# Kernel optimization log

Hardware: AMD Instinct MI355X
Metric: run time of the kernel (lower is better)

## Reference

```python
import jax, jax.numpy as jnp
import numpy as np

N = 50000          # nodes
E = 1_600_000      # edges (avg degree 32)
F = 64             # num_features == hidden dim of every layer
R = 5              # num_rel (edge ratings)
B = 4              # num_base (basis decomposition)
L = 4              # number of RGCN layers (dim=[64,64,64,64])
K = 2048           # nodes with x[:,0]==1 (target user/item nodes)


def setup_inputs() -> dict:
    key = jax.random.key(0)
    ks = jax.random.split(key, 10)
    x = jax.random.normal(ks[0], (N, F), dtype=jnp.float32)
    target_idx = jnp.arange(K, dtype=jnp.int32)
    # mark exactly K target nodes: x[:,0] == 1 iff node index < K
    col0 = (jnp.arange(N) < K).astype(jnp.float32)
    x = x.at[:, 0].set(col0)
    edge_index = jax.random.randint(ks[1], (2, E), 0, N, dtype=jnp.int32)
    edge_type = jax.random.randint(ks[2], (E,), 0, R, dtype=jnp.int32)
    s = 1.0 / np.sqrt(F)
    bases = jax.random.normal(ks[3], (L, B, F, F), dtype=jnp.float32) * s
    comps = jax.random.normal(ks[4], (L, R, B), dtype=jnp.float32) * (1.0 / np.sqrt(B))
    roots = jax.random.normal(ks[5], (L, F, F), dtype=jnp.float32) * s
    biases = jnp.zeros((L, F), dtype=jnp.float32)
    w1 = jax.random.normal(ks[6], (2 * L * F, 128), dtype=jnp.float32) * (1.0 / np.sqrt(2 * L * F))
    b1 = jnp.zeros((128,), dtype=jnp.float32)
    w2 = jax.random.normal(ks[7], (128, 1), dtype=jnp.float32) * (1.0 / np.sqrt(128))
    b2 = jnp.zeros((1,), dtype=jnp.float32)
    return {"x": x, "edge_index": edge_index, "edge_type": edge_type,
            "target_idx": target_idx, "bases": bases, "comps": comps,
            "roots": roots, "biases": biases, "w1": w1, "b1": b1,
            "w2": w2, "b2": b2}


def _rgcn_layer(x, src, dst, etype, bases_l, comp_l, root_l, bias_l):
    # basis decomposition: W_r = sum_b comp[r,b] * bases[b]   -> [R, in, out]
    W = jnp.einsum('rb,bio->rio', comp_l, bases_l)
    # transform every node under every relation, then gather per edge
    H = jnp.einsum('ni,rio->rno', x, W)          # [R, N, out]
    m = H[etype, src]                            # [E, out] per-edge messages
    # per-(target node, relation) MEAN aggregation (PyG RGCNConv semantics)
    seg = dst * R + etype                        # [E]
    sums = jax.ops.segment_sum(m, seg, num_segments=N * R)
    cnts = jax.ops.segment_sum(jnp.ones((m.shape[0],), dtype=x.dtype), seg,
                               num_segments=N * R)
    mean = sums / jnp.maximum(cnts, 1.0)[:, None]
    agg = mean.reshape(N, R, -1).sum(axis=1)     # sum over relations
    return agg + x @ root_l + bias_l


def reference(x, edge_index, edge_type, target_idx, bases, comps, roots,
              biases, w1, b1, w2, b2):
    # inference mode: edge dropout / feature dropout are identity
    src, dst = edge_index[0], edge_index[1]
    h = x
    h_i = []
    for l in range(L):
        h = jnp.tanh(_rgcn_layer(h, src, dst, edge_type,
                                 bases[l], comps[l], roots[l], biases[l]))
        h_i.append(h)
    h_cat = jnp.concatenate(h_i, axis=1)         # [N, sum(dim)] = [N, 256]
    # u and i masks are identical in the source (x[:,0]==1); target_idx holds
    # exactly those node indices, so index gather == boolean mask selection.
    sel = h_cat[target_idx]                      # [K, 256]
    feat = jnp.concatenate([sel, sel], axis=1)   # [K, 512]
    hid = jax.nn.relu(feat @ w1 + b1)
    out = hid @ w2 + b2
    return out[:, 0]
```

## Files before the change

kernel.cpp:

```cpp
#include <hip/hip_runtime.h>
#include <hip/hip_bf16.h>

#define Nn 50000
#define Ee 1600000
#define Ff 64
#define Rr 5
#define Bb 4
#define Ll 4
#define Kk 2048
#define NBK 196
#define SEGB 1280
#define MsegP (NBK*SEGB)
#define NT32 1563
#define NCH ((Ee+8191)/8192)
#define WTSL (12*4*64*8)

typedef __attribute__((ext_vector_type(8))) short short8;
typedef __attribute__((ext_vector_type(4))) float v4f;

static __device__ __forceinline__ unsigned short f2b(float f){
  unsigned u = __float_as_uint(f);
  unsigned r = (u + 0x7fffu + ((u>>16)&1u)) >> 16;
  return (unsigned short)r;
}
static __device__ __forceinline__ unsigned packbf(float lo, float hi){
  return (unsigned)f2b(lo) | ((unsigned)f2b(hi) << 16);
}
static __device__ __forceinline__ float2 unpackbf(unsigned u){
  return make_float2(__uint_as_float(u << 16), __uint_as_float(u & 0xffff0000u));
}
static __device__ __forceinline__ void acc8(float* A, uint4 g){
  float2 f;
  f=unpackbf(g.x); A[0]+=f.x; A[1]+=f.y;
  f=unpackbf(g.y); A[2]+=f.x; A[3]+=f.y;
  f=unpackbf(g.z); A[4]+=f.x; A[5]+=f.y;
  f=unpackbf(g.w); A[6]+=f.x; A[7]+=f.y;
}

#define GATH4(B, MR) { \
  int i0 = __shfl((int)(MR), grp8 + ((B)&7) + 0, 64); \
  int i1 = __shfl((int)(MR), grp8 + ((B)&7) + 1, 64); \
  int i2 = __shfl((int)(MR), grp8 + ((B)&7) + 2, 64); \
  int i3 = __shfl((int)(MR), grp8 + ((B)&7) + 3, 64); \
  i0 = ((B)+0 < deg) ? i0 : Nn; \
  i1 = ((B)+1 < deg) ? i1 : Nn; \
  i2 = ((B)+2 < deg) ? i2 : Nn; \
  i3 = ((B)+3 < deg) ? i3 : Nn; \
  uint4 g0 = *(const uint4*)&h2[(size_t)i0*32 + li*4]; \
  uint4 g1 = *(const uint4*)&h2[(size_t)i1*32 + li*4]; \
  uint4 g2 = *(const uint4*)&h2[(size_t)i2*32 + li*4]; \
  uint4 g3 = *(const uint4*)&h2[(size_t)i3*32 + li*4]; \
  acc8(A, g0); acc8(A, g1); acc8(A, g2); acc8(A, g3); }

static __device__ __forceinline__ void seg_gather(int s, int deg, unsigned m0, unsigned m1,
    float* A, int grp8, int li, const unsigned short* __restrict__ srcs,
    const unsigned* __restrict__ h2)
{
  int dmax = deg;
  dmax = max(dmax, __shfl_xor(dmax, 8, 64));
  dmax = max(dmax, __shfl_xor(dmax, 16, 64));
  dmax = max(dmax, __shfl_xor(dmax, 32, 64));
  GATH4(0, m0)
  if (dmax > 4)  GATH4(4, m0)
  if (dmax > 8)  GATH4(8, m1)
  if (dmax > 12) GATH4(12, m1)
  if (dmax > 16){
    for (int j = 16; j < dmax; j++){
      unsigned u = srcs[s + j];
      int id = (j < deg) ? (int)u : Nn;
      uint4 g = *(const uint4*)&h2[(size_t)id*32 + li*4];
      acc8(A, g);
    }
  }
}

#define XB_B 6250
#define IV_B (XB_B+196)
#define WE_B (IV_B+128)
#define WS_B (WE_B+48)
#define TF_B (WS_B+7)
__global__ __launch_bounds__(256) void k_setupA(const float* __restrict__ x, unsigned* __restrict__ xb,
    int* __restrict__ inv, const float* __restrict__ w1, float* __restrict__ w1e,
    const float* __restrict__ bases, const float* __restrict__ comps, const float* __restrict__ roots,
    unsigned short* __restrict__ WTs, int* __restrict__ t32f, int* __restrict__ bcnt,
    unsigned* __restrict__ hA, unsigned* __restrict__ hB)
{
  int b = blockIdx.x, t = threadIdx.x;
  if (b < XB_B){
    int idx = b*256 + t;
    int n = idx >> 5, j = idx & 31;
    float2 v = *(const float2*)&x[(size_t)n*64 + 2*j];
    xb[idx] = packbf(v.x, v.y);
  } else if (b < IV_B){
    int i = (b-XB_B)*256 + t;
    if (i < Nn) inv[i] = -1;
  } else if (b < WE_B){
    int idx = (b-IV_B)*256 + t;
    int i = idx >> 7, j = idx & 127;
    w1e[idx] = w1[i*128 + j] + w1[(i+256)*128 + j];
  } else if (b < WS_B){
    int gid = (b-WE_B)*256 + t;
    int lane = gid & 63, nb = (gid>>6)&3, idx2 = gid>>8;
    int l = idx2/12, kk = idx2 - l*12;
    int o = nb*16 + (lane & 15);
    int kbase = kk*32 + (lane>>4)*8;
    const float* basesl = bases + (size_t)l*Bb*Ff*Ff;
    const float* compsl = comps + (size_t)l*Rr*Bb;
    const float* rootsl = roots + (size_t)l*Ff*Ff;
    unsigned short* wp = WTs + (size_t)gid*8;
    #pragma unroll
    for (int j=0;j<8;j++){
      int k = kbase + j;
      float s;
      if (k < 320){
        int c = k >> 6, i = k & 63;
        s = 0.f;
        #pragma unroll
        for (int bb2=0;bb2<Bb;bb2++)
          s += compsl[c*Bb+bb2] * basesl[(bb2*Ff + i)*Ff + o];
      } else {
        s = rootsl[(k-320)*Ff + o];
      }
      wp[j] = f2b(s);
    }
  } else if (b < TF_B){
    int i = (b-WS_B)*256 + t;
    if (i < NT32) t32f[i] = 0;
  } else {
    if (t < NBK+1) bcnt[t] = 0;
    if (t < 32){
      xb[(size_t)Nn*32 + t] = 0;
      hA[(size_t)Nn*32 + t] = 0;
      hB[(size_t)Nn*32 + t] = 0;
    }
  }
}

__global__ __launch_bounds__(256) void k_setupB(const int* __restrict__ tidx, int* __restrict__ inv,
                                                int* __restrict__ t32f){
  int k = blockIdx.x*256+threadIdx.x;
  if (k < Kk){
    int n = tidx[k];
    inv[n] = k;
    t32f[n >> 5] = 1;
  }
}

__global__ __launch_bounds__(256) void k_bcnt(const int* __restrict__ ei, int* __restrict__ bcnt){
  __shared__ int h[NBK];
  int t = threadIdx.x;
  for (int i=t;i<NBK;i+=256) h[i]=0;
  __syncthreads();
  int base = blockIdx.x*8192;
  for (int i=0;i<32;i++){
    int e = base + i*256 + t;
    if (e < Ee) atomicAdd(&h[ei[Ee+e]>>8], 1);
  }
  __syncthreads();
  for (int i=t;i<NBK;i+=256) if (h[i]) atomicAdd(&bcnt[i], h[i]);
}

__global__ __launch_bounds__(256) void k_bscan(const int* __restrict__ bcnt, int* __restrict__ bbase,
                                               int* __restrict__ bfill, int* __restrict__ rowptr){
  __shared__ int s[256];
  int t = threadIdx.x;
  int v = (t < NBK) ? bcnt[t] : 0;
  s[t] = v; __syncthreads();
  #pragma unroll
  for (int off=1; off<256; off<<=1){
    int x = (t>=off) ? s[t-off] : 0;
    __syncthreads();
    s[t] += x;
    __syncthreads();
  }
  if (t < NBK){ int ex = s[t]-v; bbase[t]=ex; bfill[t]=ex; }
  if (t == 0){ bbase[NBK] = Ee; rowptr[MsegP] = Ee; }
}

__global__ __launch_bounds__(256) void k_bin(const int* __restrict__ ei, const int* __restrict__ et,
                                             int* __restrict__ bfill, unsigned* __restrict__ ebin){
  __shared__ unsigned led[8192];
  __shared__ int h[NBK], gb[NBK];
  int t = threadIdx.x;
  for (int i=t;i<NBK;i+=256) h[i]=0;
  __syncthreads();
  int base = blockIdx.x*8192;
  for (int i=0;i<32;i++){
    int e = base + i*256 + t;
    if (e < Ee){
      int src = ei[e];
      int dst = ei[Ee+e];
      int r = et[e];
      led[i*256+t] = (unsigned)src | ((unsigned)(dst&255)<<16) | ((unsigned)r<<24);
      atomicAdd(&h[dst>>8], 1);
    }
  }
  __syncthreads();
  for (int i=t;i<NBK;i+=256) if (h[i]){ gb[i] = atomicAdd(&bfill[i], h[i]); h[i] = 0; }
  __syncthreads();
  for (int i=0;i<32;i++){
    int e = base + i*256 + t;
    if (e < Ee){
      int b = ei[Ee+e]>>8;
      int off = atomicAdd(&h[b], 1);
      ebin[gb[b]+off] = led[i*256+t];
    }
  }
}

__global__ __launch_bounds__(512) void k_sort(const unsigned* __restrict__ ebin, const int* __restrict__ bbase,
                                              unsigned short* __restrict__ srcs, int* __restrict__ rowptr){
  __shared__ int cntA[SEGB], excA[SEGB];
  int b = blockIdx.x, t = threadIdx.x;
  int base = bbase[b], cnt = bbase[b+1]-base;
  for (int i=t;i<SEGB;i+=512) cntA[i]=0;
  __syncthreads();
  for (int i=t;i<cnt;i+=512){
    unsigned u = ebin[base+i];
    int segl = (int)((u>>24)&7u)*256 + (int)((u>>16)&255u);
    atomicAdd(&cntA[segl], 1);
  }
  __syncthreads();
  for (int i=t;i<SEGB;i+=512) excA[i]=cntA[i];
  __syncthreads();
  for (int off=1; off<SEGB; off<<=1){
    int i0=t, i1=t+512, i2=t+1024;
    int v0 = (i0>=off)? excA[i0-off] : 0;
    int v1 = (i1>=off)? excA[i1-off] : 0;
    int v2 = (i2<SEGB && i2>=off)? excA[i2-off] : 0;
    __syncthreads();
    excA[i0]+=v0;
    excA[i1]+=v1;
    if (i2<SEGB) excA[i2]+=v2;
    __syncthreads();
  }
  for (int i=t;i<SEGB;i+=512){
    int ex = excA[i]-cntA[i];
    excA[i] = ex;
    rowptr[b*SEGB+i] = base + ex;
    cntA[i] = 0;
  }
  __syncthreads();
  for (int i=t;i<cnt;i+=512){
    unsigned u = ebin[base+i];
    int segl = (int)((u>>24)&7u)*256 + (int)((u>>16)&255u);
    int off = atomicAdd(&cntA[segl], 1);
    srcs[base + excA[segl] + off] = (unsigned short)(u & 0xffffu);
  }
}

__global__ __launch_bounds__(256, 4) void k_fused(const unsigned short* __restrict__ srcs,
    const int* __restrict__ rowptr, const unsigned* __restrict__ h2,
    const unsigned short* __restrict__ WTsl, const float* __restrict__ bias,
    unsigned short* __restrict__ hn, const int* __restrict__ inv, float* __restrict__ sel,
    int layer, const int* __restrict__ t32f)
{
  if (layer == Ll-1 && t32f[blockIdx.x] == 0) return;
  __shared__ __align__(16) unsigned short ytile[5*32*64];
  char* yb = (char*)ytile;
  int tid = threadIdx.x;
  int grp = tid >> 3;
  int li  = tid & 7;
  int grp8 = (tid & 63) & 56;
  int d0 = blockIdx.x * 32;
  int segbase = (d0 >> 8)*SEGB + (d0 & 255) + grp;

  int p[Rr], dg[Rr];
  #pragma unroll
  for (int r=0;r<Rr;r++){
    p[r]  = rowptr[segbase + r*256];
    dg[r] = rowptr[segbase + r*256 + 1] - p[r];
  }
  unsigned b0[Rr], b1[Rr];
  #pragma unroll
  for (int r=0;r<Rr;r++){
    b0[r] = srcs[p[r] + li];
    b1[r] = srcs[p[r] + 8 + li];
  }

  #pragma unroll
  for (int r=0;r<Rr;r++){
    int deg = dg[r];
    float A[8] = {0.f,0.f,0.f,0.f,0.f,0.f,0.f,0.f};
    seg_gather(p[r], deg, b0[r], b1[r], A, grp8, li, srcs, h2);
    float sc = (deg > 0) ? 1.0f/(float)deg : 0.f;
    uint4 o;
    o.x = packbf(A[0]*sc, A[1]*sc);
    o.y = packbf(A[2]*sc, A[3]*sc);
    o.z = packbf(A[4]*sc, A[5]*sc);
    o.w = packbf(A[6]*sc, A[7]*sc);
    int tr = r*32 + grp;
    *(uint4*)(yb + ((tr*128 + li*16) ^ ((tr&7)<<4))) = o;
  }
  __syncthreads();

  int wv = tid >> 6;
  int lane = tid & 63;
  int m = lane & 15, q = lane >> 4;
  const unsigned short* wp = WTsl + (size_t)lane*8 + (size_t)wv*512;
  const char* h2c = (const char*)h2;
  int row0 = d0 + m, row1 = d0 + 16 + m;
  int row0c = (row0 < Nn) ? row0 : Nn-1;
  int row1c = (row1 < Nn) ? row1 : Nn-1;
  v4f acc0 = {0.f,0.f,0.f,0.f}, acc1 = {0.f,0.f,0.f,0.f};
  #pragma unroll
  for (int kk=0; kk<12; kk++){
    short8 a0, a1;
    if (kk < 10){
      int rb = (kk>>1)*32;
      a0 = *(const short8*)(yb + (((rb+m   )*128 + (kk&1)*64 + q*16) ^ ((m&7)<<4)));
      a1 = *(const short8*)(yb + (((rb+16+m)*128 + (kk&1)*64 + q*16) ^ ((m&7)<<4)));
    } else {
      a0 = *(const short8*)(h2c + (size_t)row0c*128 + (size_t)(kk&1)*64 + q*16);
      a1 = *(const short8*)(h2c + (size_t)row1c*128 + (size_t)(kk&1)*64 + q*16);
    }
    short8 bf = *(const short8*)(wp + (size_t)kk*2048);
    acc0 = __builtin_amdgcn_mfma_f32_16x16x32_bf16(a0, bf, acc0, 0, 0, 0);
    acc1 = __builtin_amdgcn_mfma_f32_16x16x32_bf16(a1, bf, acc1, 0, 0, 0);
  }
  float bc = bias[wv*16 + m];
  #pragma unroll
  for (int j=0;j<4;j++){
    int node0 = d0 + q*4 + j;
    int node1 = d0 + 16 + q*4 + j;
    float r0 = tanhf(acc0[j] + bc);
    float r1 = tanhf(acc1[j] + bc);
    if (node0 < Nn){
      if (layer != Ll-1) hn[(size_t)node0*64 + wv*16 + m] = f2b(r0);
      int k = inv[node0];
      if (k >= 0) sel[(size_t)k*256 + layer*64 + wv*16 + m] = r0;
    }
    if (node1 < Nn){
      if (layer != Ll-1) hn[(size_t)node1*64 + wv*16 + m] = f2b(r1);
      int k = inv[node1];
      if (k >= 0) sel[(size_t)k*256 + layer*64 + wv*16 + m] = r1;
    }
  }
}

__global__ __launch_bounds__(128) void k_mlp(const float* __restrict__ sel, const float* __restrict__ w1e,
    const float* __restrict__ b1, const float* __restrict__ w2, const float* __restrict__ b2,
    float* __restrict__ out)
{
  __shared__ float sfeat[256];
  __shared__ float partial[2];
  int k = blockIdx.x, j = threadIdx.x;
  for (int idx=j; idx<256; idx+=128) sfeat[idx] = sel[(size_t)k*256 + idx];
  __syncthreads();
  float a = b1[j];
  for (int i=0;i<256;i++) a += sfeat[i] * w1e[i*128 + j];
  a = fmaxf(a, 0.f);
  float v = a * w2[j];
  #pragma unroll
  for (int off=32; off>0; off>>=1) v += __shfl_down(v, off, 64);
  if ((j & 63) == 0) partial[j>>6] = v;
  __syncthreads();
  if (j == 0) out[k] = partial[0] + partial[1] + b2[0];
}

extern "C" void kernel_launch(void* const* d_in, const int* in_sizes, int n_in,
                              void* d_out, int out_size, void* d_ws, size_t ws_size,
                              hipStream_t stream){
  const float* x     = (const float*)d_in[0];
  const int*  ei     = (const int*)d_in[1];
  const int*  et     = (const int*)d_in[2];
  const int*  tidx   = (const int*)d_in[3];
  const float* bases = (const float*)d_in[4];
  const float* comps = (const float*)d_in[5];
  const float* roots = (const float*)d_in[6];
  const float* biases= (const float*)d_in[7];
  const float* w1    = (const float*)d_in[8];
  const float* b1    = (const float*)d_in[9];
  const float* w2    = (const float*)d_in[10];
  const float* b2    = (const float*)d_in[11];
  float* out = (float*)d_out;

  char* wsp = (char*)d_ws;
  size_t off = 0;
  auto alloc = [&](size_t bytes)->void*{ void* p = wsp + off; off += (bytes + 255) & ~size_t(255); return p; };
  unsigned* xb    = (unsigned*)alloc(sizeof(unsigned)*((size_t)Nn+1)*32);
  unsigned* hA    = (unsigned*)alloc(sizeof(unsigned)*((size_t)Nn+1)*32);
  unsigned* hB    = (unsigned*)alloc(sizeof(unsigned)*((size_t)Nn+1)*32);
  unsigned* ebin  = (unsigned*)alloc(sizeof(unsigned)*(size_t)Ee);
  int*      bcnt  = (int*)  alloc(sizeof(int)*(NBK+1));
  int*      bbase = (int*)  alloc(sizeof(int)*(NBK+1));
  int*      bfill = (int*)  alloc(sizeof(int)*(NBK));
  int*      rowptr= (int*)  alloc(sizeof(int)*(MsegP+1));
  unsigned short* srcs = (unsigned short*)alloc(sizeof(unsigned short)*((size_t)Ee+64));
  unsigned short* WTs  = (unsigned short*)alloc(sizeof(unsigned short)*(size_t)Ll*WTSL);
  float*    sel   = (float*)alloc(sizeof(float)*(size_t)Kk*256);
  float*    w1e   = (float*)alloc(sizeof(float)*256*128);
  int*      inv   = (int*)  alloc(sizeof(int)*(size_t)Nn);
  int*      t32f  = (int*)  alloc(sizeof(int)*NT32);
  (void)ws_size;

  k_setupA<<<TF_B+1, 256, 0, stream>>>(x, xb, inv, w1, w1e, bases, comps, roots,
                                       WTs, t32f, bcnt, hA, hB);
  k_setupB<<<(Kk+255)/256, 256, 0, stream>>>(tidx, inv, t32f);
  k_bcnt<<<NCH, 256, 0, stream>>>(ei, bcnt);
  k_bscan<<<1, 256, 0, stream>>>(bcnt, bbase, bfill, rowptr);
  k_bin<<<NCH, 256, 0, stream>>>(ei, et, bfill, ebin);
  k_sort<<<NBK, 512, 0, stream>>>(ebin, bbase, srcs, rowptr);

  const unsigned* hc = xb;
  unsigned* hn = hA;
  for (int l=0;l<Ll;l++){
    k_fused<<<NT32, 256, 0, stream>>>(srcs, rowptr, hc, WTs + (size_t)l*WTSL,
                                      biases + (size_t)l*Ff, (unsigned short*)hn,
                                      inv, sel, l, t32f);
    hc = hn;
    hn = (hn == hA) ? hB : hA;
  }
  k_mlp<<<Kk, 128, 0, stream>>>(sel, w1e, b1, w2, b2, out);
}
```

Before: 293.2 us.

## Fold bucket scan into bin/sort kernels and unroll segment gather loads

Merges the target-index setup with the bucket histogram kernel and removes the separate single-block scan kernel. Each k_bin block now recomputes the exclusive prefix over bucket counts, and k_sort derives its base with a block reduction, which cuts two launches from the preprocessing chain. The per-relation gather in the fused layer kernel now issues all 16 neighbour-row loads unconditionally in a software-pipelined sequence, with out-of-range slots pointing at a zero row, instead of branching on the wave-wide max degree. This exposes more memory-level parallelism, at the cost of redundant scan work per block and extra loads of the dummy row for low-degree segments.

```diff
diff --git a/kernel.cpp b/kernel.cpp
--- a/kernel.cpp
+++ b/kernel.cpp
@@ -37,43 +37,6 @@
   f=unpackbf(g.w); A[6]+=f.x; A[7]+=f.y;
 }
 
-#define GATH4(B, MR) { \
-  int i0 = __shfl((int)(MR), grp8 + ((B)&7) + 0, 64); \
-  int i1 = __shfl((int)(MR), grp8 + ((B)&7) + 1, 64); \
-  int i2 = __shfl((int)(MR), grp8 + ((B)&7) + 2, 64); \
-  int i3 = __shfl((int)(MR), grp8 + ((B)&7) + 3, 64); \
-  i0 = ((B)+0 < deg) ? i0 : Nn; \
-  i1 = ((B)+1 < deg) ? i1 : Nn; \
-  i2 = ((B)+2 < deg) ? i2 : Nn; \
-  i3 = ((B)+3 < deg) ? i3 : Nn; \
-  uint4 g0 = *(const uint4*)&h2[(size_t)i0*32 + li*4]; \
-  uint4 g1 = *(const uint4*)&h2[(size_t)i1*32 + li*4]; \
-  uint4 g2 = *(const uint4*)&h2[(size_t)i2*32 + li*4]; \
-  uint4 g3 = *(const uint4*)&h2[(size_t)i3*32 + li*4]; \
-  acc8(A, g0); acc8(A, g1); acc8(A, g2); acc8(A, g3); }
-
-static __device__ __forceinline__ void seg_gather(int s, int deg, unsigned m0, unsigned m1,
-    float* A, int grp8, int li, const unsigned short* __restrict__ srcs,
-    const unsigned* __restrict__ h2)
-{
-  int dmax = deg;
-  dmax = max(dmax, __shfl_xor(dmax, 8, 64));
-  dmax = max(dmax, __shfl_xor(dmax, 16, 64));
-  dmax = max(dmax, __shfl_xor(dmax, 32, 64));
-  GATH4(0, m0)
-  if (dmax > 4)  GATH4(4, m0)
-  if (dmax > 8)  GATH4(8, m1)
-  if (dmax > 12) GATH4(12, m1)
-  if (dmax > 16){
-    for (int j = 16; j < dmax; j++){
-      unsigned u = srcs[s + j];
-      int id = (j < deg) ? (int)u : Nn;
-      uint4 g = *(const uint4*)&h2[(size_t)id*32 + li*4];
-      acc8(A, g);
-    }
-  }
-}
-
 #define XB_B 6250
 #define IV_B (XB_B+196)
 #define WE_B (IV_B+128)
@@ -83,7 +46,7 @@
     int* __restrict__ inv, const float* __restrict__ w1, float* __restrict__ w1e,
     const float* __restrict__ bases, const float* __restrict__ comps, const float* __restrict__ roots,
     unsigned short* __restrict__ WTs, int* __restrict__ t32f, int* __restrict__ bcnt,
-    unsigned* __restrict__ hA, unsigned* __restrict__ hB)
+    int* __restrict__ bfill, unsigned* __restrict__ hA, unsigned* __restrict__ hB)
 {
   int b = blockIdx.x, t = threadIdx.x;
   if (b < XB_B){
@@ -128,6 +91,7 @@
     if (i < NT32) t32f[i] = 0;
   } else {
     if (t < NBK+1) bcnt[t] = 0;
+    if (t < NBK) bfill[t] = 0;
     if (t < 32){
       xb[(size_t)Nn*32 + t] = 0;
       hA[(size_t)Nn*32 + t] = 0;
@@ -137,52 +101,41 @@
 }
 
 __global__ __launch_bounds__(256) void k_setupB(const int* __restrict__ tidx, int* __restrict__ inv,
-                                                int* __restrict__ t32f){
-  int k = blockIdx.x*256+threadIdx.x;
-  if (k < Kk){
-    int n = tidx[k];
-    inv[n] = k;
-    t32f[n >> 5] = 1;
-  }
-}
-
-__global__ __launch_bounds__(256) void k_bcnt(const int* __restrict__ ei, int* __restrict__ bcnt){
-  __shared__ int h[NBK];
+                                                int* __restrict__ t32f, const int* __restrict__ ei,
+                                                int* __restrict__ bcnt){
+  int b = blockIdx.x;
+  if (b < 8){
+    int k = b*256 + threadIdx.x;
+    if (k < Kk){
+      int n = tidx[k];
+      inv[n] = k;
+      t32f[n >> 5] = 1;
+    }
+  } else {
+    __shared__ int h[NBK];
+    int t = threadIdx.x;
+    for (int i=t;i<NBK;i+=256) h[i]=0;
+    __syncthreads();
+    int base = (b-8)*8192;
+    for (int i=0;i<32;i++){
+      int e = base + i*256 + t;
+      if (e < Ee) atomicAdd(&h[ei[Ee+e]>>8], 1);
+    }
+    __syncthreads();
+    for (int i=t;i<NBK;i+=256) if (h[i]) atomicAdd(&bcnt[i], h[i]);
+  }
+}
+
+__global__ __launch_bounds__(256) void k_bin(const int* __restrict__ ei, const int* __restrict__ et,
+                                             const int* __restrict__ bcnt, int* __restrict__ bfill,
+                                             unsigned* __restrict__ ebin){
+  __shared__ unsigned led[8192];
+  __shared__ int h[NBK], gb[NBK];
+  __shared__ int ex[256];
   int t = threadIdx.x;
   for (int i=t;i<NBK;i+=256) h[i]=0;
-  __syncthreads();
-  int base = blockIdx.x*8192;
-  for (int i=0;i<32;i++){
-    int e = base + i*256 + t;
-    if (e < Ee) atomicAdd(&h[ei[Ee+e]>>8], 1);
-  }
-  __syncthreads();
-  for (int i=t;i<NBK;i+=256) if (h[i]) atomicAdd(&bcnt[i], h[i]);
-}
-
-__global__ __launch_bounds__(256) void k_bscan(const int* __restrict__ bcnt, int* __restrict__ bbase,
-                                               int* __restrict__ bfill, int* __restrict__ rowptr){
-  __shared__ int s[256];
-  int t = threadIdx.x;
   int v = (t < NBK) ? bcnt[t] : 0;
-  s[t] = v; __syncthreads();
-  #pragma unroll
-  for (int off=1; off<256; off<<=1){
-    int x = (t>=off) ? s[t-off] : 0;
-    __syncthreads();
-    s[t] += x;
-    __syncthreads();
-  }
-  if (t < NBK){ int ex = s[t]-v; bbase[t]=ex; bfill[t]=ex; }
-  if (t == 0){ bbase[NBK] = Ee; rowptr[MsegP] = Ee; }
-}
-
-__global__ __launch_bounds__(256) void k_bin(const int* __restrict__ ei, const int* __restrict__ et,
-                                             int* __restrict__ bfill, unsigned* __restrict__ ebin){
-  __shared__ unsigned led[8192];
-  __shared__ int h[NBK], gb[NBK];
-  int t = threadIdx.x;
-  for (int i=t;i<NBK;i+=256) h[i]=0;
+  ex[t] = v;
   __syncthreads();
   int base = blockIdx.x*8192;
   for (int i=0;i<32;i++){
@@ -196,23 +149,41 @@
     }
   }
   __syncthreads();
-  for (int i=t;i<NBK;i+=256) if (h[i]){ gb[i] = atomicAdd(&bfill[i], h[i]); h[i] = 0; }
+  #pragma unroll
+  for (int off=1; off<256; off<<=1){
+    int x = (t>=off) ? ex[t-off] : 0;
+    __syncthreads();
+    ex[t] += x;
+    __syncthreads();
+  }
+  if (t < NBK && h[t]){ gb[t] = ex[t] - v + atomicAdd(&bfill[t], h[t]); }
+  if (t < NBK) h[t] = 0;
   __syncthreads();
   for (int i=0;i<32;i++){
     int e = base + i*256 + t;
     if (e < Ee){
-      int b = ei[Ee+e]>>8;
-      int off = atomicAdd(&h[b], 1);
-      ebin[gb[b]+off] = led[i*256+t];
-    }
-  }
-}
-
-__global__ __launch_bounds__(512) void k_sort(const unsigned* __restrict__ ebin, const int* __restrict__ bbase,
+      int b2 = ei[Ee+e]>>8;
+      int off = atomicAdd(&h[b2], 1);
+      ebin[gb[b2]+off] = led[i*256+t];
+    }
+  }
+}
+
+__global__ __launch_bounds__(512) void k_sort(const unsigned* __restrict__ ebin, const int* __restrict__ bcnt,
                                               unsigned short* __restrict__ srcs, int* __restrict__ rowptr){
   __shared__ int cntA[SEGB], excA[SEGB];
+  __shared__ int red[512];
   int b = blockIdx.x, t = threadIdx.x;
-  int base = bbase[b], cnt = bbase[b+1]-base;
+  red[t] = (t < b) ? bcnt[t] : 0;
+  __syncthreads();
+  #pragma unroll
+  for (int off=256; off>0; off>>=1){
+    if (t < off) red[t] += red[t+off];
+    __syncthreads();
+  }
+  int base = red[0];
+  int cnt = bcnt[b];
+  if (b == 0 && t == 0) rowptr[MsegP] = Ee;
   for (int i=t;i<SEGB;i+=512) cntA[i]=0;
   __syncthreads();
   for (int i=t;i<cnt;i+=512){
@@ -248,6 +219,8 @@
     srcs[base + excA[segl] + off] = (unsigned short)(u & 0xffffu);
   }
 }
+
+#define LDROW(IDX) (*(const uint4*)&h2[(size_t)(IDX)*32 + li*4])
 
 __global__ __launch_bounds__(256, 4) void k_fused(const unsigned short* __restrict__ srcs,
     const int* __restrict__ rowptr, const unsigned* __restrict__ h2,
@@ -281,8 +254,31 @@
   #pragma unroll
   for (int r=0;r<Rr;r++){
     int deg = dg[r];
+    int id[16];
+    #pragma unroll
+    for (int j=0;j<16;j++){
+      int vsh = __shfl((int)((j<8)? b0[r] : b1[r]), grp8 + (j&7), 64);
+      id[j] = (j < deg) ? vsh : Nn;
+    }
     float A[8] = {0.f,0.f,0.f,0.f,0.f,0.f,0.f,0.f};
-    seg_gather(p[r], deg, b0[r], b1[r], A, grp8, li, srcs, h2);
+    uint4 g0=LDROW(id[0]), g1=LDROW(id[1]), g2=LDROW(id[2]), g3=LDROW(id[3]),
+          g4=LDROW(id[4]), g5=LDROW(id[5]), g6=LDROW(id[6]), g7=LDROW(id[7]);
+    acc8(A,g0); g0=LDROW(id[ 8]);
+    acc8(A,g1); g1=LDROW(id[ 9]);
+    acc8(A,g2); g2=LDROW(id[10]);
+    acc8(A,g3); g3=LDROW(id[11]);
+    acc8(A,g4); g4=LDROW(id[12]);
+    acc8(A,g5); g5=LDROW(id[13]);
+    acc8(A,g6); g6=LDROW(id[14]);
+    acc8(A,g7); g7=LDROW(id[15]);
+    acc8(A,g0); acc8(A,g1); acc8(A,g2); acc8(A,g3);
+    acc8(A,g4); acc8(A,g5); acc8(A,g6); acc8(A,g7);
+    if (deg > 16){
+      for (int j=16;j<deg;j++){
+        uint4 gt = LDROW((int)srcs[p[r]+j]);
+        acc8(A, gt);
+      }
+    }
     float sc = (deg > 0) ? 1.0f/(float)deg : 0.f;
     uint4 o;
     o.x = packbf(A[0]*sc, A[1]*sc);
@@ -383,7 +379,6 @@
   unsigned* hB    = (unsigned*)alloc(sizeof(unsigned)*((size_t)Nn+1)*32);
   unsigned* ebin  = (unsigned*)alloc(sizeof(unsigned)*(size_t)Ee);
   int*      bcnt  = (int*)  alloc(sizeof(int)*(NBK+1));
-  int*      bbase = (int*)  alloc(sizeof(int)*(NBK+1));
   int*      bfill = (int*)  alloc(sizeof(int)*(NBK));
   int*      rowptr= (int*)  alloc(sizeof(int)*(MsegP+1));
   unsigned short* srcs = (unsigned short*)alloc(sizeof(unsigned short)*((size_t)Ee+64));
@@ -395,12 +390,10 @@
   (void)ws_size;
 
   k_setupA<<<TF_B+1, 256, 0, stream>>>(x, xb, inv, w1, w1e, bases, comps, roots,
-                                       WTs, t32f, bcnt, hA, hB);
-  k_setupB<<<(Kk+255)/256, 256, 0, stream>>>(tidx, inv, t32f);
-  k_bcnt<<<NCH, 256, 0, stream>>>(ei, bcnt);
-  k_bscan<<<1, 256, 0, stream>>>(bcnt, bbase, bfill, rowptr);
-  k_bin<<<NCH, 256, 0, stream>>>(ei, et, bfill, ebin);
-  k_sort<<<NBK, 512, 0, stream>>>(ebin, bbase, srcs, rowptr);
+                                       WTs, t32f, bcnt, bfill, hA, hB);
+  k_setupB<<<8+NCH, 256, 0, stream>>>(tidx, inv, t32f, ei, bcnt);
+  k_bin<<<NCH, 256, 0, stream>>>(ei, et, bcnt, bfill, ebin);
+  k_sort<<<NBK, 512, 0, stream>>>(ebin, bcnt, srcs, rowptr);
 
   const unsigned* hc = xb;
   unsigned* hn = hA;
```

Result: faster. 280.7 us (-4.3%).
